# Performance work log

Measured on AMD Instinct MI355X. Metric: run time of the kernel, lower is better.

The kernel has to match this reference:

```python
import jax, jax.numpy as jnp
import numpy as np

B, S, D, H, DK, DV, DO = 2, 2048, 1024, 16, 64, 64, 1024


def setup_inputs() -> dict:
    key = jax.random.key(0)
    k0, k1, k2, k3, k4 = jax.random.split(key, 5)
    x = jax.random.normal(k0, (B, S, D), dtype=jnp.float32)
    # Stacked per-head projection weights (original uses H separate Linear(bias=False));
    # stored as [H, D, d_head] so q = x @ Wq[h] per head.
    Wq = jax.random.normal(k1, (H, D, DK), dtype=jnp.float32) * 0.02
    Wk = jax.random.normal(k2, (H, D, DK), dtype=jnp.float32) * 0.02
    Wv = jax.random.normal(k3, (H, D, DV), dtype=jnp.float32) * 0.02
    # Output projection Linear(dim_v*num_heads, dim_out, bias=False), stored [H*DV, DO]
    Wo = jax.random.normal(k4, (H * DV, DO), dtype=jnp.float32) * 0.02
    return {"x": x, "Wq": Wq, "Wk": Wk, "Wv": Wv, "Wo": Wo}


def reference(x, Wq, Wk, Wv, Wo):
    # Cross-head batched version of the per-head Python loop (same math).
    q = jnp.einsum('bsd,hde->bhse', x, Wq)  # [B,H,S,DK]
    k = jnp.einsum('bsd,hde->bhse', x, Wk)  # [B,H,S,DK]
    v = jnp.einsum('bsd,hde->bhse', x, Wv)  # [B,H,S,DV]
    scale = 1.0 / jnp.sqrt(jnp.asarray(k.shape[-1], dtype=x.dtype))
    scores = jnp.einsum('bhqe,bhke->bhqk', q, k) * scale  # [B,H,S,S]
    attn = jax.nn.softmax(scores, axis=-1)
    o = jnp.einsum('bhqk,bhke->bhqe', attn, v)  # [B,H,S,DV]
    # concat heads along feature dim (head order preserved)
    o = jnp.transpose(o, (0, 2, 1, 3)).reshape(o.shape[0], o.shape[2], -1)  # [B,S,H*DV]
    return o @ Wo  # [B,S,DO]
```

## Files before the change

kernel.cpp:

```cpp
#include <hip/hip_runtime.h>

typedef __bf16 bf16;
typedef __attribute__((ext_vector_type(8))) short short8;
typedef __attribute__((ext_vector_type(4))) short short4v;
typedef __attribute__((ext_vector_type(4))) float floatx4;

#define DEVINL __device__ __forceinline__

DEVINL void gll16(const void* g, void* l) {
  __builtin_amdgcn_global_load_lds((const __attribute__((address_space(1))) void*)g,
                                   (__attribute__((address_space(3))) void*)l, 16, 0, 0);
}

DEVINL float fast_exp2(float x) { return __builtin_amdgcn_exp2f(x); }

#define QSCALE 0.18033688011112042f

__global__ __launch_bounds__(256) void prep_all(const float* __restrict__ x,
                                                const float* __restrict__ Wq,
                                                const float* __restrict__ Wk,
                                                const float* __restrict__ Wv,
                                                const float* __restrict__ Wo,
                                                bf16* __restrict__ x_bf,
                                                bf16* __restrict__ WbigT,
                                                bf16* __restrict__ WoT) {
  __shared__ float tile[64][65];
  int bid = blockIdx.x;
  if (bid < 2048) {
    int i = (bid * 256 + threadIdx.x) * 8;
    float4 a = *(const float4*)(x + i);
    float4 b = *(const float4*)(x + i + 4);
    union { bf16 h[8]; short8 s; } u;
    u.h[0] = (bf16)a.x; u.h[1] = (bf16)a.y; u.h[2] = (bf16)a.z; u.h[3] = (bf16)a.w;
    u.h[4] = (bf16)b.x; u.h[5] = (bf16)b.y; u.h[6] = (bf16)b.z; u.h[7] = (bf16)b.w;
    *(short8*)(x_bf + i) = u.s;
    return;
  }
  int t = bid - 2048;
  int which = t >> 8;
  t &= 255;
  const float* in;
  bf16* out;
  int C, tilesC, tilesPerBatch;
  long inStride;
  if (which < 3) {
    in = which == 0 ? Wq : (which == 1 ? Wk : Wv);
    out = WbigT + (long)which * 1024 * 1024;
    C = 64; tilesC = 1; tilesPerBatch = 16; inStride = 65536;
  } else {
    in = Wo; out = WoT;
    C = 1024; tilesC = 16; tilesPerBatch = 256; inStride = 0;
  }
  int batch = t / tilesPerBatch;
  int tt = t % tilesPerBatch;
  int ri = tt / tilesC, ci = tt % tilesC;
  const float* src = in + batch * inStride;
  bf16* dst = out + batch * (long)65536 * (which < 3 ? 1 : 0);
  int tx = threadIdx.x & 63, ty = threadIdx.x >> 6;
#pragma unroll
  for (int i = 0; i < 16; i++) {
    int r = ty + i * 4;
    tile[r][tx] = src[(long)(ri * 64 + r) * C + ci * 64 + tx];
  }
  __syncthreads();
#pragma unroll
  for (int i = 0; i < 16; i++) {
    int c = ty + i * 4;
    dst[(long)(ci * 64 + c) * 1024 + ri * 64 + tx] = (bf16)tile[tx][c];
  }
}

__global__ __launch_bounds__(512, 2) void gemm256_qkv(const bf16* __restrict__ A,
                                                      const bf16* __restrict__ BT,
                                                      bf16* __restrict__ q_ws,
                                                      bf16* __restrict__ k_ws,
                                                      bf16* __restrict__ v_ws) {
  extern __shared__ char lds[];
  int swz = (blockIdx.x & 7) * 24 + (blockIdx.x >> 3);
  int bm = swz / 12, bn = swz % 12;
  int tid = threadIdx.x, lane = tid & 63, wid = tid >> 6;
  int wm = wid >> 2, wn = wid & 3;
  int ql = lane & 15, g = lane >> 4;
  int sw = (ql & 7) << 4;
  int hB = wn >> 1;
  char* ldsA = lds;
  char* ldsB = lds + 65536;

  const char* Abase = (const char*)A + (long)bm * 256 * 2048;
  const char* Bbase = (const char*)BT + (long)bn * 256 * 2048;
  int scb = ((tid & 7) * 16) ^ (((tid >> 3) & 7) << 4);

  floatx4 acc[8][4] = {};
  short8 aF[4], bF[4];

#define STG(dst0, src0, kt_, h_) do {                                              \
    _Pragma("unroll") for (int j_ = 0; j_ < 2; j_++)                               \
      gll16((src0) + (long)((h_) * 128 + j_ * 64 + (tid >> 3)) * 2048              \
                   + (kt_) * 128 + scb,                                            \
            (dst0) + ((kt_) & 1) * 32768 + (h_) * 16384 + j_ * 8192 + wid * 1024); \
  } while (0)
#define LDA(slot_, frh_, kk_) do {                                                 \
    _Pragma("unroll") for (int j_ = 0; j_ < 4; j_++)                               \
      aF[j_] = *(const short8*)(ldsA + (slot_) * 32768 + wm * 16384 +              \
               (((frh_) * 4 + j_) * 16 + ql) * 128 + (((kk_) * 64 + g * 16) ^ sw));\
  } while (0)
#define LDB(slot_, kk_) do {                                                       \
    _Pragma("unroll") for (int f_ = 0; f_ < 4; f_++)                               \
      bF[f_] = *(const short8*)(ldsB + (slot_) * 32768 + hB * 16384 +              \
               ((wn & 1) * 64 + f_ * 16 + ql) * 128 + (((kk_) * 64 + g * 16) ^ sw));\
  } while (0)
#define MFMA16(frh_) do {                                                          \
    __builtin_amdgcn_s_setprio(1);                                                 \
    _Pragma("unroll") for (int j_ = 0; j_ < 4; j_++)                               \
      _Pragma("unroll") for (int f_ = 0; f_ < 4; f_++)                             \
        acc[(frh_) * 4 + j_][f_] = __builtin_amdgcn_mfma_f32_16x16x32_bf16(        \
            aF[j_], bF[f_], acc[(frh_) * 4 + j_][f_], 0, 0, 0);                    \
    __builtin_amdgcn_s_setprio(0);                                                 \
  } while (0)
#define BAR __builtin_amdgcn_s_barrier()
#define LG0 asm volatile("s_waitcnt lgkmcnt(0)" ::: "memory")

  STG(ldsB, Bbase, 0, 0); STG(ldsB, Bbase, 0, 1);
  STG(ldsA, Abase, 0, 0); STG(ldsA, Abase, 0, 1);
  STG(ldsB, Bbase, 1, 0);

  for (int it = 0; it < 8; it++) {
    int b1 = 2 * it + 1, a2 = 2 * it + 2, b2 = 2 * it + 3;
    bool more = it < 7;
    asm volatile("s_waitcnt vmcnt(2)" ::: "memory");
    BAR;
    LDA(0, 0, 0); LDB(0, 0);
    STG(ldsA, Abase, b1, 0);
    BAR; LG0; MFMA16(0); BAR;
    LDA(0, 1, 0);
    STG(ldsA, Abase, b1, 1);
    BAR; LG0; MFMA16(1); BAR;
    LDA(0, 0, 1); LDB(0, 1);
    STG(ldsB, Bbase, b1, 1);
    BAR; LG0; MFMA16(0); BAR;
    LDA(0, 1, 1);
    if (more) STG(ldsB, Bbase, a2, 0);
    BAR; LG0; MFMA16(1); BAR;
    if (more) { asm volatile("s_waitcnt vmcnt(2)" ::: "memory"); }
    else      { asm volatile("s_waitcnt vmcnt(0)" ::: "memory"); }
    BAR;
    LDA(1, 0, 0); LDB(1, 0);
    if (more) STG(ldsB, Bbase, a2, 1);
    BAR; LG0; MFMA16(0); BAR;
    LDA(1, 1, 0);
    if (more) STG(ldsA, Abase, a2, 0);
    BAR; LG0; MFMA16(1); BAR;
    LDA(1, 0, 1); LDB(1, 1);
    if (more) STG(ldsA, Abase, a2, 1);
    BAR; LG0; MFMA16(0); BAR;
    LDA(1, 1, 1);
    if (more) STG(ldsB, Bbase, b2, 0);
    BAR; LG0; MFMA16(1); BAR;
  }
#undef STG
#undef LDA
#undef LDB
#undef MFMA16
#undef BAR
#undef LG0

  if (bn < 8) {
    bf16* dst = (bn < 4) ? q_ws : k_ws;
    float scale = (bn < 4) ? QSCALE : 1.0f;
#pragma unroll
    for (int fr = 0; fr < 8; fr++)
#pragma unroll
      for (int fc = 0; fc < 4; fc++)
#pragma unroll
        for (int i = 0; i < 4; i++) {
          int r = bm * 256 + wm * 128 + fr * 16 + g * 4 + i;
          int c = bn * 256 + wn * 64 + fc * 16 + ql;
          int b = r >> 11, s = r & 2047;
          int h = (c >> 6) & 15, e = c & 63;
          long bh = (long)b * 16 + h;
          dst[(bh * 2048 + s) * 64 + e] = (bf16)(acc[fr][fc][i] * scale);
        }
  } else {
#pragma unroll
    for (int fr = 0; fr < 8; fr++)
#pragma unroll
      for (int fc = 0; fc < 4; fc++) {
        int local_c = wn * 64 + fc * 16 + ql;
        int ls0 = wm * 128 + fr * 16 + g * 4;
        int s6 = ls0 & 63;
        int sp = (ls0 & ~63) | (s6 & 35) | ((s6 & 12) << 1) | ((s6 & 16) >> 2);
        union { bf16 hh[4]; short4v s4; } u;
#pragma unroll
        for (int i = 0; i < 4; i++) u.hh[i] = (bf16)acc[fr][fc][i];
        *(short4v*)(lds + local_c * 512 + ((sp * 2) ^ ((local_c & 7) << 4))) = u.s4;
      }
    __syncthreads();
    int b = bm >> 3;
    long sbase = (long)(bm & 7) * 256;
#pragma unroll
    for (int j = 0; j < 16; j++) {
      int local_c = wid * 32 + j * 2 + (lane >> 5);
      int chunk = lane & 31;
      int cg = bn * 256 + local_c;
      int h = (cg >> 6) & 15, e = cg & 63;
      long bh = (long)b * 16 + h;
      char* dstp = (char*)v_ws + ((bh * 64 + e) * 2048 + sbase) * 2 + chunk * 16;
      *(short8*)dstp = *(const short8*)(lds + local_c * 512 + ((chunk * 16) ^ ((local_c & 7) << 4)));
    }
  }
}

__global__ __launch_bounds__(256) void gemm_out(const bf16* __restrict__ A,
                                                const bf16* __restrict__ BT,
                                                float* __restrict__ Cout,
                                                int N, int gridN) {
  int cpx = gridDim.x >> 3;
  int swz = (blockIdx.x & 7) * cpx + (blockIdx.x >> 3);
  int bm = swz / gridN, bn = swz % gridN;
  __shared__ char lds[32768];
  char* ldsA = lds;
  char* ldsB = lds + 16384;
  int tid = threadIdx.x;
  int lane = tid & 63, wid = tid >> 6;
  int wr = wid >> 1, wc = wid & 1;
  floatx4 acc[4][4] = {};
  const long ldAB = 2048;
  const char* Abase = (const char*)A + (long)bm * 128 * ldAB;
  const char* Bbase = (const char*)BT + (long)bn * 128 * ldAB;

  for (int kt = 0; kt < 16; kt++) {
#pragma unroll
    for (int q = 0; q < 4; q++) {
      int r = q * 32 + (tid >> 3);
      int cb = ((tid & 7) * 16) ^ ((r & 7) << 4);
      gll16(Abase + (long)r * ldAB + kt * 128 + cb, ldsA + q * 4096 + wid * 1024);
      gll16(Bbase + (long)r * ldAB + kt * 128 + cb, ldsB + q * 4096 + wid * 1024);
    }
    asm volatile("s_waitcnt vmcnt(0)" ::: "memory");
    __syncthreads();
#pragma unroll
    for (int kk = 0; kk < 2; kk++) {
      short8 a[4], b[4];
#pragma unroll
      for (int mi = 0; mi < 4; mi++) {
        int row = wr * 64 + mi * 16 + (lane & 15);
        int col = (kk * 64 + (lane >> 4) * 16) ^ ((row & 7) << 4);
        a[mi] = *(const short8*)(ldsA + row * 128 + col);
      }
#pragma unroll
      for (int ni = 0; ni < 4; ni++) {
        int row = wc * 64 + ni * 16 + (lane & 15);
        int col = (kk * 64 + (lane >> 4) * 16) ^ ((row & 7) << 4);
        b[ni] = *(const short8*)(ldsB + row * 128 + col);
      }
#pragma unroll
      for (int mi = 0; mi < 4; mi++)
#pragma unroll
        for (int ni = 0; ni < 4; ni++)
          acc[mi][ni] = __builtin_amdgcn_mfma_f32_16x16x32_bf16(a[mi], b[ni], acc[mi][ni], 0, 0, 0);
    }
    __syncthreads();
  }

#pragma unroll
  for (int mi = 0; mi < 4; mi++)
#pragma unroll
    for (int ni = 0; ni < 4; ni++)
#pragma unroll
      for (int i = 0; i < 4; i++) {
        int r = bm * 128 + wr * 64 + mi * 16 + (lane >> 4) * 4 + i;
        int c = bn * 128 + wc * 64 + ni * 16 + (lane & 15);
        Cout[(long)r * N + c] = acc[mi][ni][i];
      }
}

__global__ __launch_bounds__(512, 2) void attn_kernel(const bf16* __restrict__ q_ws,
                                                      const bf16* __restrict__ k_ws,
                                                      const bf16* __restrict__ v_ws,
                                                      bf16* __restrict__ obuf) {
  int wgid = ((blockIdx.x & 7) << 5) + (blockIdx.x >> 3);
  int qt = wgid & 7;
  int bh = wgid >> 3;
  int b = bh >> 4, h = bh & 15;
  __shared__ char lds[65536];
  char* kbuf = lds;
  char* vbuf = lds + 32768;
  int tid = threadIdx.x, lane = tid & 63, wid = tid >> 6;
  int ql = lane & 15, g = lane >> 4;

  const char* kbase = (const char*)k_ws + (long)bh * 2048 * 128;
  const char* vbase = (const char*)v_ws + (long)bh * 64 * 4096;

  int srow = wid * 8 + (lane >> 3);
  int scb = ((lane & 7) * 16) ^ (((lane >> 3) & 7) << 4);

#define STAGE(t_) do {                                                              \
    gll16(kbase + ((long)(t_) * 64 + srow) * 128 + scb,                             \
          kbuf + ((t_) & 3) * 8192 + wid * 1024);                                   \
    gll16(vbase + (long)srow * 4096 + (long)(t_) * 128 + scb,                       \
          vbuf + ((t_) & 3) * 8192 + wid * 1024);                                   \
  } while (0)

#define WAIT2_BAR do {                                                              \
    asm volatile("s_waitcnt vmcnt(2)" ::: "memory");                                \
    __builtin_amdgcn_s_barrier();                                                   \
    asm volatile("" ::: "memory");                                                  \
  } while (0)

  int sw = (ql & 7) << 4;
  int fof0 = ql * 128 + ((g * 16) ^ sw);
  int fof1 = ql * 128 + ((64 + g * 16) ^ sw);

  const bf16* qrowL = q_ws + ((long)bh * 2048 + qt * 256 + wid * 32 + ql) * 64 + 8 * g;
  short8 qL0 = *(const short8*)(qrowL);
  short8 qL1 = *(const short8*)(qrowL + 32);
  short8 qH0 = *(const short8*)(qrowL + 1024);
  short8 qH1 = *(const short8*)(qrowL + 1024 + 32);

  union { bf16 hh[8]; short8 s; } uo1;
#pragma unroll
  for (int i = 0; i < 8; i++) uo1.hh[i] = (bf16)1.0f;
  const short8 ones = uo1.s;

  floatx4 lL = {}, lH = {};
  floatx4 oL[4] = {}, oH[4] = {};
  floatx4 saL[4], saH[4];
  short8 pbL[2], pbH[2];

#define QKSTEP(kc) do {                                                             \
    __builtin_amdgcn_s_setprio(1);                                                  \
    _Pragma("unroll") for (int t_ = 0; t_ < 4; t_++) {                              \
      short8 kf = *(const short8*)((kc) + fof0 + t_ * 2048);                        \
      saL[t_] = __builtin_amdgcn_mfma_f32_16x16x32_bf16(kf, qL0, (floatx4){}, 0, 0, 0); \
      saH[t_] = __builtin_amdgcn_mfma_f32_16x16x32_bf16(kf, qH0, (floatx4){}, 0, 0, 0); \
    }                                                                               \
    _Pragma("unroll") for (int t_ = 0; t_ < 4; t_++) {                              \
      short8 kf = *(const short8*)((kc) + fof1 + t_ * 2048);                        \
      saL[t_] = __builtin_amdgcn_mfma_f32_16x16x32_bf16(kf, qL1, saL[t_], 0, 0, 0); \
      saH[t_] = __builtin_amdgcn_mfma_f32_16x16x32_bf16(kf, qH1, saH[t_], 0, 0, 0); \
    }                                                                               \
    __builtin_amdgcn_s_setprio(0);                                                  \
  } while (0)

#define SM_HALF(sa, pb, l_acc, o_acc) do {                                          \
    if (__builtin_expect(l_acc[0] > 1e30f, 0)) {                                    \
      const float c_ = 7.8886091e-31f;                                  \
      _Pragma("unroll") for (int t_ = 0; t_ < 4; t_++)                              \
        _Pragma("unroll") for (int i_ = 0; i_ < 4; i_++) o_acc[t_][i_] *= c_;       \
      _Pragma("unroll") for (int i_ = 0; i_ < 4; i_++) l_acc[i_] *= c_;             \
    }                                                                               \
    _Pragma("unroll") for (int kk_ = 0; kk_ < 2; kk_++) {                           \
      union { bf16 hh[8]; short8 s; } up_;                                          \
      _Pragma("unroll") for (int r_ = 0; r_ < 4; r_++)                              \
        up_.hh[r_] = (bf16)fast_exp2(sa[2 * kk_][r_]);                              \
      _Pragma("unroll") for (int r_ = 0; r_ < 4; r_++)                              \
        up_.hh[4 + r_] = (bf16)fast_exp2(sa[2 * kk_ + 1][r_]);                      \
      pb[kk_] = up_.s;                                                              \
    }                                                                               \
  } while (0)

#define SMSTEP do { SM_HALF(saL, pbL, lL, oL); SM_HALF(saH, pbH, lH, oH); } while (0)

#define PVSTEP(vc) do {                                                             \
    __builtin_amdgcn_s_setprio(1);                                                  \
    lL = __builtin_amdgcn_mfma_f32_16x16x32_bf16(ones, pbL[0], lL, 0, 0, 0);        \
    lL = __builtin_amdgcn_mfma_f32_16x16x32_bf16(ones, pbL[1], lL, 0, 0, 0);        \
    lH = __builtin_amdgcn_mfma_f32_16x16x32_bf16(ones, pbH[0], lH, 0, 0, 0);        \
    lH = __builtin_amdgcn_mfma_f32_16x16x32_bf16(ones, pbH[1], lH, 0, 0, 0);        \
    _Pragma("unroll") for (int t_ = 0; t_ < 4; t_++) {                              \
      short8 vf = *(const short8*)((vc) + fof0 + t_ * 2048);                        \
      oL[t_] = __builtin_amdgcn_mfma_f32_16x16x32_bf16(vf, pbL[0], oL[t_], 0, 0, 0);\
      oH[t_] = __builtin_amdgcn_mfma_f32_16x16x32_bf16(vf, pbH[0], oH[t_], 0, 0, 0);\
    }                                                                               \
    _Pragma("unroll") for (int t_ = 0; t_ < 4; t_++) {                              \
      short8 vf = *(const short8*)((vc) + fof1 + t_ * 2048);                        \
      oL[t_] = __builtin_amdgcn_mfma_f32_16x16x32_bf16(vf, pbL[1], oL[t_], 0, 0, 0);\
      oH[t_] = __builtin_amdgcn_mfma_f32_16x16x32_bf16(vf, pbH[1], oH[t_], 0, 0, 0);\
    }                                                                               \
    __builtin_amdgcn_s_setprio(0);                                                  \
  } while (0)

  STAGE(0); STAGE(1);
  WAIT2_BAR;
  QKSTEP(kbuf + 0 * 8192);
  STAGE(2);
  SMSTEP;
  WAIT2_BAR;
  STAGE(3);
  QKSTEP(kbuf + 1 * 8192);

  for (int t = 1; t <= 29; t++) {
    PVSTEP(vbuf + ((t - 1) & 3) * 8192);
    SMSTEP;
    WAIT2_BAR;
    if (t <= 28) STAGE(t + 3);
    QKSTEP(kbuf + ((t + 1) & 3) * 8192);
  }

  PVSTEP(vbuf + (29 & 3) * 8192);
  SMSTEP;
  __syncthreads();
  QKSTEP(kbuf + (31 & 3) * 8192);

  PVSTEP(vbuf + (30 & 3) * 8192);
  SMSTEP;
  PVSTEP(vbuf + (31 & 3) * 8192);

#undef STAGE
#undef WAIT2_BAR
#undef QKSTEP
#undef SM_HALF
#undef SMSTEP
#undef PVSTEP

  {
    float invL = 1.f / lL[0];
    float invH = 1.f / lH[0];
    int s = qt * 256 + wid * 32 + ql;
    bf16* orowL = obuf + ((long)b * 2048 + s) * 1024 + h * 64;
    bf16* orowH = orowL + 16 * 1024;
#pragma unroll
    for (int t = 0; t < 4; t++) {
      union { bf16 hh[4]; short4v s4; } uo;
#pragma unroll
      for (int r = 0; r < 4; r++) uo.hh[r] = (bf16)(oL[t][r] * invL);
      *(short4v*)(orowL + t * 16 + 4 * g) = uo.s4;
#pragma unroll
      for (int r = 0; r < 4; r++) uo.hh[r] = (bf16)(oH[t][r] * invH);
      *(short4v*)(orowH + t * 16 + 4 * g) = uo.s4;
    }
  }
}

extern "C" void kernel_launch(void* const* d_in, const int* in_sizes, int n_in,
                              void* d_out, int out_size, void* d_ws, size_t ws_size,
                              hipStream_t stream) {
  const float* x  = (const float*)d_in[0];
  const float* Wq = (const float*)d_in[1];
  const float* Wk = (const float*)d_in[2];
  const float* Wv = (const float*)d_in[3];
  const float* Wo = (const float*)d_in[4];
  float* out = (float*)d_out;

  char* ws = (char*)d_ws;
  bf16* x_bf  = (bf16*)(ws);
  bf16* WbigT = (bf16*)(ws + 8388608);
  bf16* WoT   = (bf16*)(ws + 14680064);
  bf16* q_ws  = (bf16*)(ws + 16777216);
  bf16* k_ws  = (bf16*)(ws + 25165824);
  bf16* v_ws  = (bf16*)(ws + 33554432);
  bf16* obuf  = (bf16*)(ws + 41943040);

  hipFuncSetAttribute((const void*)gemm256_qkv,
                      hipFuncAttributeMaxDynamicSharedMemorySize, 131072);

  prep_all<<<3072, 256, 0, stream>>>(x, Wq, Wk, Wv, Wo, x_bf, WbigT, WoT);
  gemm256_qkv<<<192, 512, 131072, stream>>>(x_bf, WbigT, q_ws, k_ws, v_ws);
  attn_kernel<<<256, 512, 0, stream>>>(q_ws, k_ws, v_ws, obuf);
  gemm_out<<<256, 256, 0, stream>>>(obuf, WoT, out, 1024, 8);
}
```

Baseline: 102.9 us.

## Split attention KV range across two wave groups and double-buffer output GEMM

The attention kernel now runs 1024 threads per block. Two groups of 8 waves each process half of the key/value sequence with their own LDS buffers. The partial outputs and row sums are then merged through LDS; this relies on the softmax being computed without a running max. Separately, the output GEMM now prefetches the next K tile into a second LDS buffer before computing the current one, overlapping loads with MFMA work. The costs are twice the LDS per attention block, an extra reduction step, and a larger LDS footprint in the GEMM.

Measured after the change: 100.3 us (median of 2 runs). 2.5% less time.

```diff
diff --git a/kernel.cpp b/kernel.cpp
--- a/kernel.cpp
+++ b/kernel.cpp
@@ -217,27 +217,37 @@
   int cpx = gridDim.x >> 3;
   int swz = (blockIdx.x & 7) * cpx + (blockIdx.x >> 3);
   int bm = swz / gridN, bn = swz % gridN;
-  __shared__ char lds[32768];
-  char* ldsA = lds;
-  char* ldsB = lds + 16384;
+  __shared__ char lds[65536];
   int tid = threadIdx.x;
   int lane = tid & 63, wid = tid >> 6;
   int wr = wid >> 1, wc = wid & 1;
   floatx4 acc[4][4] = {};
-  const long ldAB = 2048;
-  const char* Abase = (const char*)A + (long)bm * 128 * ldAB;
-  const char* Bbase = (const char*)BT + (long)bn * 128 * ldAB;
-
+  const char* Abase = (const char*)A + (long)bm * 128 * 2048;
+  const char* Bbase = (const char*)BT + (long)bn * 128 * 2048;
+  int scb = ((tid & 7) * 16) ^ (((tid >> 3) & 7) << 4);
+
+#define OSTG(kt_) do {                                                             \
+    char* la_ = lds + ((kt_) & 1) * 16384;                                         \
+    char* lb_ = lds + 32768 + ((kt_) & 1) * 16384;                                 \
+    _Pragma("unroll") for (int q_ = 0; q_ < 4; q_++) {                             \
+      gll16(Abase + (long)(q_ * 32 + (tid >> 3)) * 2048 + (kt_) * 128 + scb,       \
+            la_ + q_ * 4096 + wid * 1024);                                         \
+      gll16(Bbase + (long)(q_ * 32 + (tid >> 3)) * 2048 + (kt_) * 128 + scb,       \
+            lb_ + q_ * 4096 + wid * 1024);                                         \
+    }                                                                              \
+  } while (0)
+
+  OSTG(0);
   for (int kt = 0; kt < 16; kt++) {
-#pragma unroll
-    for (int q = 0; q < 4; q++) {
-      int r = q * 32 + (tid >> 3);
-      int cb = ((tid & 7) * 16) ^ ((r & 7) << 4);
-      gll16(Abase + (long)r * ldAB + kt * 128 + cb, ldsA + q * 4096 + wid * 1024);
-      gll16(Bbase + (long)r * ldAB + kt * 128 + cb, ldsB + q * 4096 + wid * 1024);
+    if (kt < 15) {
+      OSTG(kt + 1);
+      asm volatile("s_waitcnt vmcnt(8)" ::: "memory");
+    } else {
+      asm volatile("s_waitcnt vmcnt(0)" ::: "memory");
     }
-    asm volatile("s_waitcnt vmcnt(0)" ::: "memory");
-    __syncthreads();
+    __builtin_amdgcn_s_barrier();
+    char* la = lds + (kt & 1) * 16384;
+    char* lb = lds + 32768 + (kt & 1) * 16384;
 #pragma unroll
     for (int kk = 0; kk < 2; kk++) {
       short8 a[4], b[4];
@@ -245,13 +255,13 @@
       for (int mi = 0; mi < 4; mi++) {
         int row = wr * 64 + mi * 16 + (lane & 15);
         int col = (kk * 64 + (lane >> 4) * 16) ^ ((row & 7) << 4);
-        a[mi] = *(const short8*)(ldsA + row * 128 + col);
+        a[mi] = *(const short8*)(la + row * 128 + col);
       }
 #pragma unroll
       for (int ni = 0; ni < 4; ni++) {
         int row = wc * 64 + ni * 16 + (lane & 15);
         int col = (kk * 64 + (lane >> 4) * 16) ^ ((row & 7) << 4);
-        b[ni] = *(const short8*)(ldsB + row * 128 + col);
+        b[ni] = *(const short8*)(lb + row * 128 + col);
       }
 #pragma unroll
       for (int mi = 0; mi < 4; mi++)
@@ -259,8 +269,9 @@
         for (int ni = 0; ni < 4; ni++)
           acc[mi][ni] = __builtin_amdgcn_mfma_f32_16x16x32_bf16(a[mi], b[ni], acc[mi][ni], 0, 0, 0);
     }
-    __syncthreads();
-  }
+    __builtin_amdgcn_s_barrier();
+  }
+#undef OSTG
 
 #pragma unroll
   for (int mi = 0; mi < 4; mi++)
@@ -274,31 +285,32 @@
       }
 }
 
-__global__ __launch_bounds__(512, 2) void attn_kernel(const bf16* __restrict__ q_ws,
-                                                      const bf16* __restrict__ k_ws,
-                                                      const bf16* __restrict__ v_ws,
-                                                      bf16* __restrict__ obuf) {
+__global__ __launch_bounds__(1024, 4) void attn_kernel(const bf16* __restrict__ q_ws,
+                                                       const bf16* __restrict__ k_ws,
+                                                       const bf16* __restrict__ v_ws,
+                                                       bf16* __restrict__ obuf) {
+  extern __shared__ char lds[];
   int wgid = ((blockIdx.x & 7) << 5) + (blockIdx.x >> 3);
   int qt = wgid & 7;
   int bh = wgid >> 3;
   int b = bh >> 4, h = bh & 15;
-  __shared__ char lds[65536];
-  char* kbuf = lds;
-  char* vbuf = lds + 32768;
   int tid = threadIdx.x, lane = tid & 63, wid = tid >> 6;
+  int grp = wid >> 3, w8 = wid & 7;
   int ql = lane & 15, g = lane >> 4;
-
-  const char* kbase = (const char*)k_ws + (long)bh * 2048 * 128;
-  const char* vbase = (const char*)v_ws + (long)bh * 64 * 4096;
-
-  int srow = wid * 8 + (lane >> 3);
+  char* kbuf = lds + grp * 65536;
+  char* vbuf = kbuf + 32768;
+
+  const char* kbase = (const char*)k_ws + (long)bh * 2048 * 128 + (long)grp * 16 * 64 * 128;
+  const char* vbase = (const char*)v_ws + (long)bh * 64 * 4096 + (long)grp * 16 * 128;
+
+  int srow = w8 * 8 + (lane >> 3);
   int scb = ((lane & 7) * 16) ^ (((lane >> 3) & 7) << 4);
 
 #define STAGE(t_) do {                                                              \
     gll16(kbase + ((long)(t_) * 64 + srow) * 128 + scb,                             \
-          kbuf + ((t_) & 3) * 8192 + wid * 1024);                                   \
+          kbuf + ((t_) & 3) * 8192 + w8 * 1024);                                    \
     gll16(vbase + (long)srow * 4096 + (long)(t_) * 128 + scb,                       \
-          vbuf + ((t_) & 3) * 8192 + wid * 1024);                                   \
+          vbuf + ((t_) & 3) * 8192 + w8 * 1024);                                    \
   } while (0)
 
 #define WAIT2_BAR do {                                                              \
@@ -311,7 +323,7 @@
   int fof0 = ql * 128 + ((g * 16) ^ sw);
   int fof1 = ql * 128 + ((64 + g * 16) ^ sw);
 
-  const bf16* qrowL = q_ws + ((long)bh * 2048 + qt * 256 + wid * 32 + ql) * 64 + 8 * g;
+  const bf16* qrowL = q_ws + ((long)bh * 2048 + qt * 256 + w8 * 32 + ql) * 64 + 8 * g;
   short8 qL0 = *(const short8*)(qrowL);
   short8 qL1 = *(const short8*)(qrowL + 32);
   short8 qH0 = *(const short8*)(qrowL + 1024);
@@ -389,22 +401,22 @@
   STAGE(3);
   QKSTEP(kbuf + 1 * 8192);
 
-  for (int t = 1; t <= 29; t++) {
+  for (int t = 1; t <= 13; t++) {
     PVSTEP(vbuf + ((t - 1) & 3) * 8192);
     SMSTEP;
     WAIT2_BAR;
-    if (t <= 28) STAGE(t + 3);
+    if (t <= 12) STAGE(t + 3);
     QKSTEP(kbuf + ((t + 1) & 3) * 8192);
   }
 
-  PVSTEP(vbuf + (29 & 3) * 8192);
+  PVSTEP(vbuf + (13 & 3) * 8192);
   SMSTEP;
   __syncthreads();
-  QKSTEP(kbuf + (31 & 3) * 8192);
-
-  PVSTEP(vbuf + (30 & 3) * 8192);
+  QKSTEP(kbuf + (15 & 3) * 8192);
+
+  PVSTEP(vbuf + (14 & 3) * 8192);
   SMSTEP;
-  PVSTEP(vbuf + (31 & 3) * 8192);
+  PVSTEP(vbuf + (15 & 3) * 8192);
 
 #undef STAGE
 #undef WAIT2_BAR
@@ -413,20 +425,35 @@
 #undef SMSTEP
 #undef PVSTEP
 
-  {
-    float invL = 1.f / lL[0];
-    float invH = 1.f / lH[0];
-    int s = qt * 256 + wid * 32 + ql;
+  __syncthreads();
+  if (grp == 1) {
+    char* pbase = lds + 65536 + w8 * 8192;
+#pragma unroll
+    for (int t = 0; t < 4; t++) {
+      *(floatx4*)(pbase + (t * 2 + 0) * 1024 + lane * 16) = oL[t];
+      *(floatx4*)(pbase + (t * 2 + 1) * 1024 + lane * 16) = oH[t];
+    }
+    *(float2*)(lds + w8 * 512 + lane * 8) = make_float2(lL[0], lH[0]);
+  }
+  __syncthreads();
+  if (grp == 0) {
+    float2 lp = *(const float2*)(lds + w8 * 512 + lane * 8);
+    const char* pbase = lds + 65536 + w8 * 8192;
+    float invL = 1.f / (lL[0] + lp.x);
+    float invH = 1.f / (lH[0] + lp.y);
+    int s = qt * 256 + w8 * 32 + ql;
     bf16* orowL = obuf + ((long)b * 2048 + s) * 1024 + h * 64;
     bf16* orowH = orowL + 16 * 1024;
 #pragma unroll
     for (int t = 0; t < 4; t++) {
+      floatx4 aL = *(const floatx4*)(pbase + (t * 2 + 0) * 1024 + lane * 16);
+      floatx4 aH = *(const floatx4*)(pbase + (t * 2 + 1) * 1024 + lane * 16);
       union { bf16 hh[4]; short4v s4; } uo;
 #pragma unroll
-      for (int r = 0; r < 4; r++) uo.hh[r] = (bf16)(oL[t][r] * invL);
+      for (int r = 0; r < 4; r++) uo.hh[r] = (bf16)((oL[t][r] + aL[r]) * invL);
       *(short4v*)(orowL + t * 16 + 4 * g) = uo.s4;
 #pragma unroll
-      for (int r = 0; r < 4; r++) uo.hh[r] = (bf16)(oH[t][r] * invH);
+      for (int r = 0; r < 4; r++) uo.hh[r] = (bf16)((oH[t][r] + aH[r]) * invH);
       *(short4v*)(orowH + t * 16 + 4 * g) = uo.s4;
     }
   }
@@ -453,9 +480,11 @@
 
   hipFuncSetAttribute((const void*)gemm256_qkv,
                       hipFuncAttributeMaxDynamicSharedMemorySize, 131072);
+  hipFuncSetAttribute((const void*)attn_kernel,
+                      hipFuncAttributeMaxDynamicSharedMemorySize, 131072);
 
   prep_all<<<3072, 256, 0, stream>>>(x, Wq, Wk, Wv, Wo, x_bf, WbigT, WoT);
   gemm256_qkv<<<192, 512, 131072, stream>>>(x_bf, WbigT, q_ws, k_ws, v_ws);
-  attn_kernel<<<256, 512, 0, stream>>>(q_ws, k_ws, v_ws, obuf);
+  attn_kernel<<<256, 1024, 131072, stream>>>(q_ws, k_ws, v_ws, obuf);
   gemm_out<<<256, 256, 0, stream>>>(obuf, WoT, out, 1024, 8);
 }
```
